# Kernel optimization log

Hardware: AMD Instinct MI355X
Metric: run time of the kernel (lower is better)

The kernel has to match this reference:

```python
import jax, jax.numpy as jnp
import numpy as np

N_NODES = 50000

def cheb_conv(x, edge_index, W, b):
    # PyG ChebConv, K=2, normalization='sym', lambda_max=2.0 (default):
    # scaled Laplacian L_hat = (2/lambda_max)*L - I = -D^{-1/2} A D^{-1/2} (zero diag).
    # Tx_0 = x, Tx_1 = L_hat @ x ; out = Tx_0 @ W[0] + Tx_1 @ W[1] + b
    src, dst = edge_index[0], edge_index[1]
    ones = jnp.ones(src.shape[0], x.dtype)
    deg = jax.ops.segment_sum(ones, src, num_segments=N_NODES)
    dinv = jnp.where(deg > 0, 1.0 / jnp.sqrt(deg), 0.0)
    norm = -dinv[src] * dinv[dst]                                   # [E]
    tx1 = jax.ops.segment_sum(x[src] * norm[:, None], dst, num_segments=N_NODES)
    return x @ W[0] + tx1 @ W[1] + b

def setup_inputs() -> dict:
    key = jax.random.key(0)
    ks = jax.random.split(key, 12)
    IN, OUT, E, P = 128, 2, 800000, 400000
    return {
        "x": jax.random.normal(ks[0], (N_NODES, IN), jnp.float32),
        "edge_index": jax.random.randint(ks[1], (2, E), 0, N_NODES),
        "E_pos": jax.random.randint(ks[2], (2, P), 0, N_NODES),
        "neg_edge_index": jax.random.randint(ks[3], (2, P), 0, N_NODES),
        "W1": jax.random.normal(ks[4], (2, IN, 300), jnp.float32) * 0.05,
        "b1": jnp.zeros((300,), jnp.float32),
        "W2": jax.random.normal(ks[5], (2, 300, 100), jnp.float32) * 0.05,
        "b2": jnp.zeros((100,), jnp.float32),
        "W3": jax.random.normal(ks[6], (2, 100, OUT), jnp.float32) * 0.05,
        "b3": jnp.zeros((OUT,), jnp.float32),
        "lin1_W": jax.random.normal(ks[7], (100, IN), jnp.float32) * 0.05,
        "lin1_b": jnp.zeros((100,), jnp.float32),
        "lin2_W": jax.random.normal(ks[8], (100, IN), jnp.float32) * 0.05,
        "lin2_b": jnp.zeros((100,), jnp.float32),
        "c1": jnp.full((1,), 0.5, jnp.float32),
        "c2": jnp.full((1,), 0.5, jnp.float32),
    }

def reference(x, edge_index, E_pos, neg_edge_index, W1, b1, W2, b2, W3, b3,
              lin1_W, lin1_b, lin2_W, lin2_b, c1, c2):
    # eval mode: F.dropout and dropout_edge are identity
    x0 = x
    h = jax.nn.relu(cheb_conv(x0, edge_index, W1, b1))
    x1 = jax.nn.relu(cheb_conv(h, edge_index, W2, b2))
    x2 = x1 + jax.nn.relu(x0 @ lin1_W.T + lin1_b)
    z = x1 + jax.nn.relu(x0 @ lin2_W.T + lin2_b)
    pos_score = jnp.sum(z[E_pos[0]] * z[E_pos[1]], axis=1)              # [P]
    pos_loss = -jnp.mean(jnp.log(jax.nn.sigmoid(pos_score) + 1e-15))
    neg_score = jnp.sum(z[neg_edge_index[0]] * z[neg_edge_index[1]], axis=1)
    neg_loss = -jnp.mean(jnp.log(1.0 - jax.nn.sigmoid(neg_score) + 1e-15))
    r_loss = pos_loss + neg_loss
    out = cheb_conv(x2, edge_index, W3, b3)                             # [N, out_channels]
    return (out, r_loss, c1, c2)
```

## Files before the change

kernel.cpp:

```cpp
#include <hip/hip_runtime.h>
#include <math.h>


typedef unsigned short ushort_t;
typedef unsigned char u8;
typedef __attribute__((ext_vector_type(8))) __bf16 bf16x8;
typedef __attribute__((ext_vector_type(8))) short s16x8;
typedef __attribute__((ext_vector_type(4))) float f32x4;
typedef __attribute__((ext_vector_type(2))) float f32x2;

#define NB_H 256
#define HW 12500
#define PW 25000

__device__ __forceinline__ f32x4 mfma16x16x32(s16x8 a, s16x8 b, f32x4 c) {
  return __builtin_amdgcn_mfma_f32_16x16x32_bf16(
      __builtin_bit_cast(bf16x8, a), __builtin_bit_cast(bf16x8, b), c, 0, 0, 0);
}
__device__ __forceinline__ ushort_t f2bf(float f) {
  union { float f; unsigned u; } c; c.f = f;
  unsigned r = (c.u + 0x7FFFu + ((c.u >> 16) & 1u)) >> 16;
  return (ushort_t)r;
}
__device__ __forceinline__ f32x2 cvt2lo(unsigned u) {
  return __builtin_amdgcn_cvt_pk_f32_fp8((int)u, false);
}
__device__ __forceinline__ f32x2 cvt2hi(unsigned u) {
  return __builtin_amdgcn_cvt_pk_f32_fp8((int)u, true);
}
__device__ __forceinline__ u8 f2fp8(float f) {
  return (u8)(__builtin_amdgcn_cvt_pk_fp8_f32(f, 0.f, 0, false) & 0xff);
}

template<int VAR, int NT, int KTOT>
__global__ __launch_bounds__(256) void gemm_mfma(
    const ushort_t* __restrict__ A0, const ushort_t* __restrict__ A1,
    const ushort_t* __restrict__ Wt,
    const float* __restrict__ bias0, const float* __restrict__ bias1,
    const float* __restrict__ x1,
    const float* __restrict__ W3c, const float* __restrict__ b3c,
    void* __restrict__ out0, void* __restrict__ out1,
    float* __restrict__ t0g, float* __restrict__ t1g, int M)
{
  constexpr int NF = NT / 32;
  __shared__ __align__(16) ushort_t As[64 * 40];
  __shared__ __align__(16) ushort_t Bs[NT * 40];
  __shared__ float w3s[400];
  const int tid  = threadIdx.x;
  const int lane = tid & 63, w = tid >> 6;
  const int m0 = blockIdx.x * 64;
  const int wm = (w & 1) * 32, wn = (w >> 1) * (NT / 2);
  if (VAR == 2) { for (int i = tid; i < 400; i += 256) w3s[i] = W3c[i]; }
  f32x4 acc[2][NF];
#pragma unroll
  for (int i = 0; i < 2; ++i)
#pragma unroll
    for (int j = 0; j < NF; ++j) acc[i][j] = (f32x4){0.f, 0.f, 0.f, 0.f};

  for (int k0 = 0; k0 < KTOT; k0 += 32) {
    {
      const int r = tid >> 2, c8 = (tid & 3) * 8;
      const int gm = m0 + r;
      uint4 v = {0u, 0u, 0u, 0u};
      if (gm < M) {
        const ushort_t* srcp;
        if (VAR == 0) srcp = (k0 < 128) ? A0 + (size_t)gm * 128 + k0 + c8
                                        : A1 + (size_t)gm * 128 + (k0 - 128) + c8;
        else if (VAR == 1) srcp = A0 + (size_t)gm * 320 + k0 + c8;
        else srcp = A0 + (size_t)gm * 128 + k0 + c8;
        v = *(const uint4*)srcp;
      }
      *(uint4*)&As[r * 40 + c8] = v;
    }
    {
      const int c8 = (tid & 3) * 8;
#pragma unroll
      for (int i = 0; i < (NT * 4 + 255) / 256; ++i) {
        const int r = (tid >> 2) + i * 64;
        if (r < NT)
          *(uint4*)&Bs[r * 40 + c8] = *(const uint4*)(Wt + (size_t)r * KTOT + k0 + c8);
      }
    }
    __syncthreads();
    s16x8 af[2], bfr[NF];
#pragma unroll
    for (int mi = 0; mi < 2; ++mi)
      af[mi] = *(const s16x8*)&As[(wm + mi * 16 + (lane & 15)) * 40 + (lane >> 4) * 8];
#pragma unroll
    for (int ni = 0; ni < NF; ++ni)
      bfr[ni] = *(const s16x8*)&Bs[(wn + ni * 16 + (lane & 15)) * 40 + (lane >> 4) * 8];
#pragma unroll
    for (int mi = 0; mi < 2; ++mi)
#pragma unroll
      for (int ni = 0; ni < NF; ++ni)
        acc[mi][ni] = mfma16x16x32(af[mi], bfr[ni], acc[mi][ni]);
    __syncthreads();
  }

  if (VAR == 2) {
#pragma unroll
    for (int mi = 0; mi < 2; ++mi)
#pragma unroll
      for (int r = 0; r < 4; ++r) {
        const int gRow = m0 + wm + mi * 16 + ((lane >> 4) << 2) + r;
        float p0 = 0.f, p1 = 0.f, p2 = 0.f, p3 = 0.f;
#pragma unroll
        for (int ni = 0; ni < NF; ++ni) {
          const int col = wn + ni * 16 + (lane & 15);
          const float v = acc[mi][ni][r];
          if (gRow < M) {
            if (col < 100) {
              const float x2v = x1[(size_t)gRow * 128 + col] + fmaxf(v + bias0[col], 0.f);
              p0 = fmaf(x2v, w3s[col * 2 + 0], p0);
              p1 = fmaf(x2v, w3s[col * 2 + 1], p1);
              p2 = fmaf(x2v, w3s[200 + col * 2 + 0], p2);
              p3 = fmaf(x2v, w3s[200 + col * 2 + 1], p3);
            } else if (col < 200) {
              const int c = col - 100;
              ((u8*)out1)[(size_t)gRow * 128 + c] =
                  f2fp8(x1[(size_t)gRow * 128 + c] + fmaxf(v + bias1[c], 0.f));
            }
          }
        }
        if (wn == 0) {
#pragma unroll
          for (int off = 8; off; off >>= 1) {
            p0 += __shfl_down(p0, off, 16);
            p1 += __shfl_down(p1, off, 16);
            p2 += __shfl_down(p2, off, 16);
            p3 += __shfl_down(p3, off, 16);
          }
          if ((lane & 15) == 0 && gRow < M) {
            t0g[(size_t)gRow * 2 + 0] = p0 + b3c[0];
            t0g[(size_t)gRow * 2 + 1] = p1 + b3c[1];
            t1g[(size_t)gRow * 2 + 0] = p2;
            t1g[(size_t)gRow * 2 + 1] = p3;
          }
        }
      }
  } else {
#pragma unroll
    for (int mi = 0; mi < 2; ++mi)
#pragma unroll
      for (int ni = 0; ni < NF; ++ni)
#pragma unroll
        for (int r = 0; r < 4; ++r) {
          const int gRow = m0 + wm + mi * 16 + ((lane >> 4) << 2) + r;
          const int col  = wn + ni * 16 + (lane & 15);
          if (gRow >= M) continue;
          const float v = acc[mi][ni][r];
          if (VAR == 0) {
            ushort_t* h = (ushort_t*)out0;
            h[(size_t)gRow * 320 + col] = (col < 300) ? f2bf(fmaxf(v + bias0[col], 0.f))
                                                      : (ushort_t)0;
          } else {
            if (col < 100) ((float*)out0)[(size_t)gRow * 128 + col] = v + bias0[col];
            else if (col < 200) ((u8*)out1)[(size_t)gRow * 128 + (col - 100)] = f2fp8(v);
          }
        }
  }
}

__global__ void pack_cvt(const float* __restrict__ x, ushort_t* __restrict__ xb,
                         u8* __restrict__ xf8, int n4,
                         const float* __restrict__ W1, const float* __restrict__ W2,
                         const float* __restrict__ l1W, const float* __restrict__ l2W,
                         ushort_t* __restrict__ W1t, ushort_t* __restrict__ W2t,
                         ushort_t* __restrict__ Wlt) {
  const int i = blockIdx.x * 256 + threadIdx.x;
  if (i < n4) {
    const float4 v = ((const float4*)x)[i];
    ushort4 o; o.x = f2bf(v.x); o.y = f2bf(v.y); o.z = f2bf(v.z); o.w = f2bf(v.w);
    ((ushort4*)xb)[i] = o;
    int p = 0;
    p = __builtin_amdgcn_cvt_pk_fp8_f32(v.x, v.y, p, false);
    p = __builtin_amdgcn_cvt_pk_fp8_f32(v.z, v.w, p, true);
    ((unsigned*)xf8)[i] = (unsigned)p;
    return;
  }
  const int j = i - n4;
  if (j < 81920) {
    const int n = j >> 8, k = j & 255;
    float v = 0.f;
    if (n < 300) v = (k < 128) ? W1[k * 300 + n] : W1[38400 + (k - 128) * 300 + n];
    W1t[j] = f2bf(v);
  } else if (j < 153600) {
    const int jj = j - 81920;
    const int n = jj / 320, k = jj - n * 320;
    float v = 0.f;
    if (n < 200 && k < 300) v = W2[(n < 100 ? 0 : 30000) + k * 100 + (n % 100)];
    W2t[jj] = f2bf(v);
  } else if (j < 182272) {
    const int jj = j - 153600;
    const int n = jj >> 7, k = jj & 127;
    float v = 0.f;
    if (n < 100) v = l1W[n * 128 + k];
    else if (n < 200) v = l2W[(n - 100) * 128 + k];
    Wlt[jj] = f2bf(v);
  }
}

__global__ __launch_bounds__(256) void hist2(
    const int* __restrict__ src, const int* __restrict__ dst, int E, int M,
    unsigned* __restrict__ partS, unsigned* __restrict__ partD,
    ushort_t* __restrict__ rank)
{
  __shared__ unsigned hist[HW];
  const int b = blockIdx.x;
  const int cs = (E + NB_H - 1) / NB_H;
  const int e0 = b * cs;
  const int e1 = (e0 + cs < E) ? e0 + cs : E;
  for (int isD = 0; isD < 2; ++isD) {
    const int* keys = isD ? dst : src;
    unsigned* part = isD ? partD : partS;
    for (int r = 0; r < 2; ++r) {
      const int klo = r * 2 * HW;
      for (int i = threadIdx.x; i < HW; i += 256) hist[i] = 0;
      __syncthreads();
      for (int e = e0 + threadIdx.x; e < e1; e += 256) {
        const int k = keys[e] - klo;
        if ((unsigned)k < (unsigned)(2 * HW)) {
          const unsigned old = atomicAdd(&hist[k >> 1], (k & 1) ? 0x10000u : 1u);
          if (isD) rank[e] = (ushort_t)((old >> ((k & 1) * 16)) & 0xffffu);
        }
      }
      __syncthreads();
      for (int i = threadIdx.x; i < HW; i += 256)
        part[(size_t)b * PW + r * HW + i] = hist[i];
      __syncthreads();
    }
  }
}

__global__ __launch_bounds__(256) void reduce_base2(
    const unsigned* __restrict__ partS, unsigned* __restrict__ partD,
    float* __restrict__ dinv, int* __restrict__ cnt, int M)
{
  const int t = blockIdx.x * 256 + threadIdx.x;
  if (t < PW) {
    const int i = t;
    unsigned ssum = 0;
    for (int b = 0; b < NB_H; b += 8) {
      unsigned v[8];
#pragma unroll
      for (int q = 0; q < 8; ++q) v[q] = partS[(size_t)(b + q) * PW + i];
#pragma unroll
      for (int q = 0; q < 8; ++q) ssum += v[q];
    }
    const int k = 2 * i;
    const unsigned s0 = ssum & 0xffffu, s1 = ssum >> 16;
    if (k < M) dinv[k] = s0 ? 1.f / sqrtf((float)s0) : 0.f;
    if (k + 1 < M) dinv[k + 1] = s1 ? 1.f / sqrtf((float)s1) : 0.f;
  } else if (t < 2 * PW) {
    const int i = t - PW;
    unsigned run = 0;
    for (int b = 0; b < NB_H; b += 8) {
      unsigned v[8], pre[8];
#pragma unroll
      for (int q = 0; q < 8; ++q) v[q] = partD[(size_t)(b + q) * PW + i];
#pragma unroll
      for (int q = 0; q < 8; ++q) { pre[q] = run; run += v[q]; }
#pragma unroll
      for (int q = 0; q < 8; ++q) partD[(size_t)(b + q) * PW + i] = pre[q];
    }
    const int k = 2 * i;
    if (k < M) cnt[k] = (int)(run & 0xffffu);
    if (k + 1 < M) cnt[k + 1] = (int)(run >> 16);
  }
}

__global__ void scan_local(const int* __restrict__ cnt, int* __restrict__ ptr,
                           int* __restrict__ bsum, int n)
{
  __shared__ int tmp[256];
  const int i = blockIdx.x * 256 + threadIdx.x;
  const int v = (i < n) ? cnt[i] : 0;
  tmp[threadIdx.x] = v;
  __syncthreads();
  for (int off = 1; off < 256; off <<= 1) {
    const int t = (threadIdx.x >= off) ? tmp[threadIdx.x - off] : 0;
    __syncthreads();
    tmp[threadIdx.x] += t;
    __syncthreads();
  }
  if (i < n) ptr[i] = tmp[threadIdx.x] - v;
  if (threadIdx.x == 255) bsum[blockIdx.x] = tmp[255];
}
__global__ void scan_bsum(int* __restrict__ bsum, int nb, float* __restrict__ accs) {
  __shared__ int tmp[256];
  if (threadIdx.x < 2) accs[threadIdx.x] = 0.f;
  const int v = (threadIdx.x < nb) ? bsum[threadIdx.x] : 0;
  tmp[threadIdx.x] = v;
  __syncthreads();
  for (int off = 1; off < 256; off <<= 1) {
    const int t = (threadIdx.x >= off) ? tmp[threadIdx.x - off] : 0;
    __syncthreads();
    tmp[threadIdx.x] += t;
    __syncthreads();
  }
  if (threadIdx.x < nb) bsum[threadIdx.x] = tmp[threadIdx.x] - v;
}
__global__ void scan_add(int* __restrict__ ptr, const int* __restrict__ bsum, int n, int E) {
  const int i = blockIdx.x * 256 + threadIdx.x;
  if (i < n) ptr[i] += bsum[blockIdx.x];
  if (i == 0) ptr[n] = E;
}

__global__ void fill_csr2(const int* __restrict__ src, const int* __restrict__ dst,
                          const float* __restrict__ dinv, const int* __restrict__ ptr,
                          const unsigned* __restrict__ base32,
                          const ushort_t* __restrict__ rank,
                          int2* __restrict__ csr, int E)
{
  const int e = blockIdx.x * 256 + threadIdx.x;
  if (e >= E) return;
  const int cs = (E + NB_H - 1) / NB_H;
  const int b = e / cs;
  const int s = src[e], d = dst[e];
  const unsigned bv = base32[(size_t)b * PW + (d >> 1)];
  const int base = (int)((bv >> ((d & 1) * 16)) & 0xffffu);
  const int pos = ptr[d] + base + (int)rank[e];
  const float w = -dinv[s] * dinv[d];
  csr[pos] = make_int2(s, __float_as_int(w));
}

#define ACCV(u, ww) { f32x2 t; \
  t = cvt2lo(u.x); a[0]  = fmaf(ww, t.x, a[0]);  a[1]  = fmaf(ww, t.y, a[1]);  \
  t = cvt2hi(u.x); a[2]  = fmaf(ww, t.x, a[2]);  a[3]  = fmaf(ww, t.y, a[3]);  \
  t = cvt2lo(u.y); a[4]  = fmaf(ww, t.x, a[4]);  a[5]  = fmaf(ww, t.y, a[5]);  \
  t = cvt2hi(u.y); a[6]  = fmaf(ww, t.x, a[6]);  a[7]  = fmaf(ww, t.y, a[7]);  \
  t = cvt2lo(u.z); a[8]  = fmaf(ww, t.x, a[8]);  a[9]  = fmaf(ww, t.y, a[9]);  \
  t = cvt2hi(u.z); a[10] = fmaf(ww, t.x, a[10]); a[11] = fmaf(ww, t.y, a[11]); \
  t = cvt2lo(u.w); a[12] = fmaf(ww, t.x, a[12]); a[13] = fmaf(ww, t.y, a[13]); \
  t = cvt2hi(u.w); a[14] = fmaf(ww, t.x, a[14]); a[15] = fmaf(ww, t.y, a[15]); }

__global__ __launch_bounds__(256) void gather128e(
    const u8* __restrict__ xf8, ushort_t* __restrict__ txb,
    const int* __restrict__ ptr, const int2* __restrict__ csr, int M)
{
  const int node = (blockIdx.x * 256 + threadIdx.x) >> 3;
  const int sub  = threadIdx.x & 7;
  if (node >= M) return;
  const int beg = ptr[node], end = ptr[node + 1];
  float a[16] = {};
  int p = beg;
  for (; p + 8 <= end; p += 8) {
    int2 e[8];
#pragma unroll
    for (int q = 0; q < 8; ++q) e[q] = csr[p + q];
    uint4 v[8];
#pragma unroll
    for (int q = 0; q < 8; ++q)
      v[q] = *(const uint4*)(xf8 + (size_t)e[q].x * 128 + sub * 16);
#pragma unroll
    for (int q = 0; q < 8; ++q) { const float wq = __int_as_float(e[q].y); ACCV(v[q], wq) }
  }
  for (; p < end; ++p) {
    const int2 eq = csr[p]; const float wq = __int_as_float(eq.y);
    const uint4 v = *(const uint4*)(xf8 + (size_t)eq.x * 128 + sub * 16);
    ACCV(v, wq)
  }
  uint4 o1, o2;
  o1.x = (unsigned)f2bf(a[0])  | ((unsigned)f2bf(a[1])  << 16);
  o1.y = (unsigned)f2bf(a[2])  | ((unsigned)f2bf(a[3])  << 16);
  o1.z = (unsigned)f2bf(a[4])  | ((unsigned)f2bf(a[5])  << 16);
  o1.w = (unsigned)f2bf(a[6])  | ((unsigned)f2bf(a[7])  << 16);
  o2.x = (unsigned)f2bf(a[8])  | ((unsigned)f2bf(a[9])  << 16);
  o2.y = (unsigned)f2bf(a[10]) | ((unsigned)f2bf(a[11]) << 16);
  o2.z = (unsigned)f2bf(a[12]) | ((unsigned)f2bf(a[13]) << 16);
  o2.w = (unsigned)f2bf(a[14]) | ((unsigned)f2bf(a[15]) << 16);
  ushort_t* dstp = txb + (size_t)node * 128 + sub * 16;
  *(uint4*)dstp = o1;
  *(uint4*)(dstp + 8) = o2;
}

__global__ __launch_bounds__(256) void gather100e_x1(
    const u8* __restrict__ Brh, float* __restrict__ Ar,
    const int* __restrict__ ptr, const int2* __restrict__ csr, int M)
{
  const int node = (blockIdx.x * 256 + threadIdx.x) >> 3;
  const int sub  = threadIdx.x & 7;
  if (node >= M) return;
  const int beg = ptr[node], end = ptr[node + 1];
  float a[16] = {};
  int p = beg;
  for (; p + 8 <= end; p += 8) {
    int2 e[8];
#pragma unroll
    for (int q = 0; q < 8; ++q) e[q] = csr[p + q];
    uint4 v[8];
#pragma unroll
    for (int q = 0; q < 8; ++q)
      v[q] = *(const uint4*)(Brh + (size_t)e[q].x * 128 + sub * 16);
#pragma unroll
    for (int q = 0; q < 8; ++q) { const float wq = __int_as_float(e[q].y); ACCV(v[q], wq) }
  }
  for (; p < end; ++p) {
    const int2 eq = csr[p]; const float wq = __int_as_float(eq.y);
    const uint4 v = *(const uint4*)(Brh + (size_t)eq.x * 128 + sub * 16);
    ACCV(v, wq)
  }
  float* dstp = Ar + (size_t)node * 128 + sub * 16;
#pragma unroll
  for (int q = 0; q < 4; ++q) {
    float4 b = *(const float4*)(dstp + q * 4);
    b.x = fmaxf(b.x + a[q * 4 + 0], 0.f);
    b.y = fmaxf(b.y + a[q * 4 + 1], 0.f);
    b.z = fmaxf(b.z + a[q * 4 + 2], 0.f);
    b.w = fmaxf(b.w + a[q * 4 + 3], 0.f);
    *(float4*)(dstp + q * 4) = b;
  }
}
#undef ACCV

__device__ __forceinline__ void maskrow(uint4& r, int sub) {
  if (sub >= 6) { r.y = 0u; r.z = 0u; r.w = 0u; if (sub == 7) r.x = 0u; }
}
#define DOTV(uu, vv, s) { f32x2 p_, q_; \
  p_ = cvt2lo(uu.x); q_ = cvt2lo(vv.x); s = fmaf(p_.x, q_.x, s); s = fmaf(p_.y, q_.y, s); \
  p_ = cvt2hi(uu.x); q_ = cvt2hi(vv.x); s = fmaf(p_.x, q_.x, s); s = fmaf(p_.y, q_.y, s); \
  p_ = cvt2lo(uu.y); q_ = cvt2lo(vv.y); s = fmaf(p_.x, q_.x, s); s = fmaf(p_.y, q_.y, s); \
  p_ = cvt2hi(uu.y); q_ = cvt2hi(vv.y); s = fmaf(p_.x, q_.x, s); s = fmaf(p_.y, q_.y, s); \
  p_ = cvt2lo(uu.z); q_ = cvt2lo(vv.z); s = fmaf(p_.x, q_.x, s); s = fmaf(p_.y, q_.y, s); \
  p_ = cvt2hi(uu.z); q_ = cvt2hi(vv.z); s = fmaf(p_.x, q_.x, s); s = fmaf(p_.y, q_.y, s); \
  p_ = cvt2lo(uu.w); q_ = cvt2lo(vv.w); s = fmaf(p_.x, q_.x, s); s = fmaf(p_.y, q_.y, s); \
  p_ = cvt2hi(uu.w); q_ = cvt2hi(vv.w); s = fmaf(p_.x, q_.x, s); s = fmaf(p_.y, q_.y, s); }

__global__ __launch_bounds__(256) void loss_fp8(
    const u8* __restrict__ zf8, const int* __restrict__ ep,
    const int* __restrict__ en, int P, float* __restrict__ acc)
{
  __shared__ float red[8];
  const int tid = threadIdx.x;
  const int lane = tid & 63, wib = tid >> 6;
  const int sub = tid & 7;
  const int slot0 = blockIdx.x * 32 + (tid >> 3);
  const int step = gridDim.x * 32;
  float tp = 0.f, tn = 0.f;
  int g = slot0;
  for (; g + 3 * step < 2 * P; g += 4 * step) {
    int neg[4], na[4], nb[4];
#pragma unroll
    for (int q = 0; q < 4; ++q) {
      const int gq = g + q * step;
      neg[q] = (gq >= P);
      const int p = neg[q] ? gq - P : gq;
      const int* ia = neg[q] ? en : ep;
      na[q] = ia[p]; nb[q] = ia[P + p];
    }
    uint4 ra[4], rb[4];
#pragma unroll
    for (int q = 0; q < 4; ++q) {
      ra[q] = *(const uint4*)(zf8 + (size_t)na[q] * 128 + sub * 16);
      rb[q] = *(const uint4*)(zf8 + (size_t)nb[q] * 128 + sub * 16);
      maskrow(ra[q], sub); maskrow(rb[q], sub);
    }
    float s[4] = {0.f, 0.f, 0.f, 0.f};
#pragma unroll
    for (int q = 0; q < 4; ++q) DOTV(ra[q], rb[q], s[q])
#pragma unroll
    for (int off = 4; off; off >>= 1) {
#pragma unroll
      for (int q = 0; q < 4; ++q) s[q] += __shfl_down(s[q], off, 8);
    }
    if (sub == 0) {
#pragma unroll
      for (int q = 0; q < 4; ++q) {
        const float sig = 1.f / (1.f + expf(-s[q]));
        if (neg[q]) tn += logf(1.f - sig + 1e-15f); else tp += logf(sig + 1e-15f);
      }
    }
  }
  for (; g < 2 * P; g += step) {
    const int neg = (g >= P);
    const int p = neg ? g - P : g;
    const int* ia = neg ? en : ep;
    const int na = ia[p], nb = ia[P + p];
    uint4 ra = *(const uint4*)(zf8 + (size_t)na * 128 + sub * 16);
    uint4 rb = *(const uint4*)(zf8 + (size_t)nb * 128 + sub * 16);
    maskrow(ra, sub); maskrow(rb, sub);
    float s = 0.f;
    DOTV(ra, rb, s)
#pragma unroll
    for (int off = 4; off; off >>= 1) s += __shfl_down(s, off, 8);
    if (sub == 0) {
      const float sig = 1.f / (1.f + expf(-s));
      if (neg) tn += logf(1.f - sig + 1e-15f); else tp += logf(sig + 1e-15f);
    }
  }
  tp += __shfl_down(tp, 32, 64); tn += __shfl_down(tn, 32, 64);
  tp += __shfl_down(tp, 16, 64); tn += __shfl_down(tn, 16, 64);
  tp += __shfl_down(tp, 8, 64);  tn += __shfl_down(tn, 8, 64);
  if (lane == 0) { red[wib] = tp; red[4 + wib] = tn; }
  __syncthreads();
  if (tid == 0) {
    atomicAdd(acc + 0, red[0] + red[1] + red[2] + red[3]);
    atomicAdd(acc + 1, red[4] + red[5] + red[6] + red[7]);
  }
}
#undef DOTV

__global__ void gather2_final(
    const float* __restrict__ t1, const float* __restrict__ t0,
    const int* __restrict__ ptr, const int2* __restrict__ csr,
    const float* __restrict__ accs,
    const float* __restrict__ c1, const float* __restrict__ c2,
    float* __restrict__ out, int M, float invP)
{
  const int i = blockIdx.x * blockDim.x + threadIdx.x;
  if (i < M) {
    float a0 = 0.f, a1 = 0.f;
    const int beg = ptr[i], end = ptr[i + 1];
    int p = beg;
    for (; p + 4 <= end; p += 4) {
      const int2 e0 = csr[p], e1 = csr[p + 1], e2 = csr[p + 2], e3 = csr[p + 3];
      const float w0 = __int_as_float(e0.y), w1 = __int_as_float(e1.y);
      const float w2 = __int_as_float(e2.y), w3 = __int_as_float(e3.y);
      const float2 v0 = *(const float2*)(t1 + (size_t)e0.x * 2);
      const float2 v1 = *(const float2*)(t1 + (size_t)e1.x * 2);
      const float2 v2 = *(const float2*)(t1 + (size_t)e2.x * 2);
      const float2 v3 = *(const float2*)(t1 + (size_t)e3.x * 2);
      a0 = fmaf(w0, v0.x, a0); a1 = fmaf(w0, v0.y, a1);
      a0 = fmaf(w1, v1.x, a0); a1 = fmaf(w1, v1.y, a1);
      a0 = fmaf(w2, v2.x, a0); a1 = fmaf(w2, v2.y, a1);
      a0 = fmaf(w3, v3.x, a0); a1 = fmaf(w3, v3.y, a1);
    }
    for (; p < end; ++p) {
      const int2 eq = csr[p]; const float wq = __int_as_float(eq.y);
      const float2 v = *(const float2*)(t1 + (size_t)eq.x * 2);
      a0 = fmaf(wq, v.x, a0); a1 = fmaf(wq, v.y, a1);
    }
    const float2 base = *(const float2*)(t0 + (size_t)i * 2);
    *(float2*)(out + (size_t)i * 2) = make_float2(base.x + a0, base.y + a1);
  }
  if (i == 0) {
    out[2 * M + 0] = -(accs[0] + accs[1]) * invP;
    out[2 * M + 1] = c1[0];
    out[2 * M + 2] = c2[0];
  }
}

extern "C" void kernel_launch(void* const* d_in, const int* in_sizes, int n_in,
                              void* d_out, int out_size, void* d_ws, size_t ws_size,
                              hipStream_t stream)
{
  const float* x   = (const float*)d_in[0];
  const int*   ei  = (const int*)d_in[1];
  const int*   ep  = (const int*)d_in[2];
  const int*   en  = (const int*)d_in[3];
  const float* W1  = (const float*)d_in[4];
  const float* b1  = (const float*)d_in[5];
  const float* W2  = (const float*)d_in[6];
  const float* b2  = (const float*)d_in[7];
  const float* W3  = (const float*)d_in[8];
  const float* b3  = (const float*)d_in[9];
  const float* l1W = (const float*)d_in[10];
  const float* l1b = (const float*)d_in[11];
  const float* l2W = (const float*)d_in[12];
  const float* l2b = (const float*)d_in[13];
  const float* c1  = (const float*)d_in[14];
  const float* c2  = (const float*)d_in[15];
  float* out = (float*)d_out;

  const int M = in_sizes[0] / 128;
  const int E = in_sizes[1] / 2;
  const int P = in_sizes[2] / 2;
  const int* src = ei;
  const int* dst = ei + E;
  const int nb_scan = (M + 255) / 256;

  float* ws = (float*)d_ws;
  size_t o = 0;
  float*    dinv = ws + o;            o += 50176;
  int*      cnt  = (int*)(ws + o);    o += (size_t)M;
  int*      ptr  = (int*)(ws + o);    o += (size_t)M + 8;
  int*      bsum = (int*)(ws + o);    o += 256;
  int2*     csr  = (int2*)(ws + o);   o += (size_t)E * 2;
  ushort_t* rank = (ushort_t*)(ws + o); o += (size_t)E / 2;
  ushort_t* xb   = (ushort_t*)(ws + o); o += (size_t)M * 64;
  u8*       xf8  = (u8*)(ws + o);     o += (size_t)M * 32;
  ushort_t* tx0b = (ushort_t*)(ws + o); o += (size_t)M * 64;
  ushort_t* W1t  = (ushort_t*)(ws + o); o += 40960;
  ushort_t* W2t  = (ushort_t*)(ws + o); o += 35840;
  ushort_t* Wlt  = (ushort_t*)(ws + o); o += 14336;
  ushort_t* h    = (ushort_t*)(ws + o); o += (size_t)M * 160;
  float*    Ar   = ws + o;            o += (size_t)M * 128;
  u8*       Brh  = (u8*)(ws + o);     o += (size_t)M * 32;
  u8*       zf8  = (u8*)(ws + o);     o += (size_t)M * 32;
  float*    t0   = ws + o;            o += (size_t)M * 2;
  float*    t1   = ws + o;            o += (size_t)M * 2;
  float*    accs = ws + o;            o += 8;
  unsigned* partS = (unsigned*)h;
  unsigned* partD = (unsigned*)Ar;

  const int n4 = M * 32;
  pack_cvt<<<(n4 + 182272 + 255) / 256, 256, 0, stream>>>(
      x, xb, xf8, n4, W1, W2, l1W, l2W, W1t, W2t, Wlt);

  hist2<<<NB_H, 256, 0, stream>>>(src, dst, E, M, partS, partD, rank);
  reduce_base2<<<(2 * PW + 255) / 256, 256, 0, stream>>>(partS, partD, dinv, cnt, M);
  scan_local<<<nb_scan, 256, 0, stream>>>(cnt, ptr, bsum, M);
  scan_bsum<<<1, 256, 0, stream>>>(bsum, nb_scan, accs);
  scan_add<<<nb_scan, 256, 0, stream>>>(ptr, bsum, M, E);
  fill_csr2<<<(E + 255) / 256, 256, 0, stream>>>(src, dst, dinv, ptr, partD, rank, csr, E);

  const int gB = (M + 63) / 64;
  const int gE8 = (M * 8 + 255) / 256;

  gather128e<<<gE8, 256, 0, stream>>>(xf8, tx0b, ptr, csr, M);
  gemm_mfma<0, 320, 256><<<gB, 256, 0, stream>>>(
      xb, tx0b, W1t, b1, nullptr, nullptr, nullptr, nullptr, h, nullptr, nullptr, nullptr, M);

  gemm_mfma<1, 224, 320><<<gB, 256, 0, stream>>>(
      h, nullptr, W2t, b2, nullptr, nullptr, nullptr, nullptr, Ar, Brh, nullptr, nullptr, M);
  gather100e_x1<<<gE8, 256, 0, stream>>>(Brh, Ar, ptr, csr, M);

  gemm_mfma<2, 224, 128><<<gB, 256, 0, stream>>>(
      xb, nullptr, Wlt, l1b, l2b, Ar , W3, b3, nullptr, zf8, t0, t1, M);

  loss_fp8<<<2048, 256, 0, stream>>>(zf8, ep, en, P, accs);

  gather2_final<<<(M + 255) / 256, 256, 0, stream>>>(t1, t0, ptr, csr,
                                                     accs, c1, c2, out, M, 1.0f / (float)P);
}
```

Measured before the change: 476.9 us.

## Split fp8 feature tables into two 64-byte column planes for cache-resident gathers

Stores the fp8 copies of x, Brh and z as two planes of 64 bytes per node instead of 128-byte rows. The sparse gathers and the loss dot-products then run as two passes, one per plane, so each pass touches half the working set and has a better chance of staying in L2/MALL. The loss is split into a partial-sum pass that writes per-pair scores and a second pass that adds the rest and applies the log-sigmoid. This adds extra kernel launches, reads the CSR and edge indices twice, and writes and reads a 2P-float scratch buffer.

```diff
diff --git a/kernel.cpp b/kernel.cpp
--- a/kernel.cpp
+++ b/kernel.cpp
@@ -50,6 +50,7 @@
   const int lane = tid & 63, w = tid >> 6;
   const int m0 = blockIdx.x * 64;
   const int wm = (w & 1) * 32, wn = (w >> 1) * (NT / 2);
+  const size_t pstride = (size_t)M * 64;
   if (VAR == 2) { for (int i = tid; i < 400; i += 256) w3s[i] = W3c[i]; }
   f32x4 acc[2][NF];
 #pragma unroll
@@ -117,7 +118,8 @@
               p3 = fmaf(x2v, w3s[200 + col * 2 + 1], p3);
             } else if (col < 200) {
               const int c = col - 100;
-              ((u8*)out1)[(size_t)gRow * 128 + c] =
+              const int pl = (c >= 64);
+              ((u8*)out1)[pl * pstride + (size_t)gRow * 64 + (c - pl * 64)] =
                   f2fp8(x1[(size_t)gRow * 128 + c] + fmaxf(v + bias1[c], 0.f));
             }
           }
@@ -155,14 +157,18 @@
                                                       : (ushort_t)0;
           } else {
             if (col < 100) ((float*)out0)[(size_t)gRow * 128 + col] = v + bias0[col];
-            else if (col < 200) ((u8*)out1)[(size_t)gRow * 128 + (col - 100)] = f2fp8(v);
+            else if (col < 200) {
+              const int c = col - 100;
+              const int pl = (c >= 64);
+              ((u8*)out1)[pl * pstride + (size_t)gRow * 64 + (c - pl * 64)] = f2fp8(v);
+            }
           }
         }
   }
 }
 
 __global__ void pack_cvt(const float* __restrict__ x, ushort_t* __restrict__ xb,
-                         u8* __restrict__ xf8, int n4,
+                         u8* __restrict__ xf8, int n4, int M,
                          const float* __restrict__ W1, const float* __restrict__ W2,
                          const float* __restrict__ l1W, const float* __restrict__ l2W,
                          ushort_t* __restrict__ W1t, ushort_t* __restrict__ W2t,
@@ -175,7 +181,10 @@
     int p = 0;
     p = __builtin_amdgcn_cvt_pk_fp8_f32(v.x, v.y, p, false);
     p = __builtin_amdgcn_cvt_pk_fp8_f32(v.z, v.w, p, true);
-    ((unsigned*)xf8)[i] = (unsigned)p;
+    const int row = i >> 5, g = i & 31;
+    const int col = g * 4;
+    const int pl = col >> 6, off = col & 63;
+    *(unsigned*)(xf8 + (size_t)pl * M * 64 + (size_t)row * 64 + off) = (unsigned)p;
     return;
   }
   const int j = i - n4;
@@ -334,12 +343,13 @@
   t = cvt2lo(u.w); a[12] = fmaf(ww, t.x, a[12]); a[13] = fmaf(ww, t.y, a[13]); \
   t = cvt2hi(u.w); a[14] = fmaf(ww, t.x, a[14]); a[15] = fmaf(ww, t.y, a[15]); }
 
-__global__ __launch_bounds__(256) void gather128e(
-    const u8* __restrict__ xf8, ushort_t* __restrict__ txb,
+template<int PLANE>
+__global__ __launch_bounds__(256) void gather128p(
+    const u8* __restrict__ xp, ushort_t* __restrict__ txb,
     const int* __restrict__ ptr, const int2* __restrict__ csr, int M)
 {
-  const int node = (blockIdx.x * 256 + threadIdx.x) >> 3;
-  const int sub  = threadIdx.x & 7;
+  const int node = (blockIdx.x * 256 + threadIdx.x) >> 2;
+  const int sub  = threadIdx.x & 3;
   if (node >= M) return;
   const int beg = ptr[node], end = ptr[node + 1];
   float a[16] = {};
@@ -351,13 +361,13 @@
     uint4 v[8];
 #pragma unroll
     for (int q = 0; q < 8; ++q)
-      v[q] = *(const uint4*)(xf8 + (size_t)e[q].x * 128 + sub * 16);
+      v[q] = *(const uint4*)(xp + (size_t)e[q].x * 64 + sub * 16);
 #pragma unroll
     for (int q = 0; q < 8; ++q) { const float wq = __int_as_float(e[q].y); ACCV(v[q], wq) }
   }
   for (; p < end; ++p) {
     const int2 eq = csr[p]; const float wq = __int_as_float(eq.y);
-    const uint4 v = *(const uint4*)(xf8 + (size_t)eq.x * 128 + sub * 16);
+    const uint4 v = *(const uint4*)(xp + (size_t)eq.x * 64 + sub * 16);
     ACCV(v, wq)
   }
   uint4 o1, o2;
@@ -369,17 +379,18 @@
   o2.y = (unsigned)f2bf(a[10]) | ((unsigned)f2bf(a[11]) << 16);
   o2.z = (unsigned)f2bf(a[12]) | ((unsigned)f2bf(a[13]) << 16);
   o2.w = (unsigned)f2bf(a[14]) | ((unsigned)f2bf(a[15]) << 16);
-  ushort_t* dstp = txb + (size_t)node * 128 + sub * 16;
+  ushort_t* dstp = txb + (size_t)node * 128 + PLANE * 64 + sub * 16;
   *(uint4*)dstp = o1;
   *(uint4*)(dstp + 8) = o2;
 }
 
-__global__ __launch_bounds__(256) void gather100e_x1(
-    const u8* __restrict__ Brh, float* __restrict__ Ar,
+template<int PLANE>
+__global__ __launch_bounds__(256) void gather100p_x1(
+    const u8* __restrict__ Bp, float* __restrict__ Ar,
     const int* __restrict__ ptr, const int2* __restrict__ csr, int M)
 {
-  const int node = (blockIdx.x * 256 + threadIdx.x) >> 3;
-  const int sub  = threadIdx.x & 7;
+  const int node = (blockIdx.x * 256 + threadIdx.x) >> 2;
+  const int sub  = threadIdx.x & 3;
   if (node >= M) return;
   const int beg = ptr[node], end = ptr[node + 1];
   float a[16] = {};
@@ -391,16 +402,16 @@
     uint4 v[8];
 #pragma unroll
     for (int q = 0; q < 8; ++q)
-      v[q] = *(const uint4*)(Brh + (size_t)e[q].x * 128 + sub * 16);
+      v[q] = *(const uint4*)(Bp + (size_t)e[q].x * 64 + sub * 16);
 #pragma unroll
     for (int q = 0; q < 8; ++q) { const float wq = __int_as_float(e[q].y); ACCV(v[q], wq) }
   }
   for (; p < end; ++p) {
     const int2 eq = csr[p]; const float wq = __int_as_float(eq.y);
-    const uint4 v = *(const uint4*)(Brh + (size_t)eq.x * 128 + sub * 16);
+    const uint4 v = *(const uint4*)(Bp + (size_t)eq.x * 64 + sub * 16);
     ACCV(v, wq)
   }
-  float* dstp = Ar + (size_t)node * 128 + sub * 16;
+  float* dstp = Ar + (size_t)node * 128 + PLANE * 64 + sub * 16;
 #pragma unroll
   for (int q = 0; q < 4; ++q) {
     float4 b = *(const float4*)(dstp + q * 4);
@@ -413,9 +424,6 @@
 }
 #undef ACCV
 
-__device__ __forceinline__ void maskrow(uint4& r, int sub) {
-  if (sub >= 6) { r.y = 0u; r.z = 0u; r.w = 0u; if (sub == 7) r.x = 0u; }
-}
 #define DOTV(uu, vv, s) { f32x2 p_, q_; \
   p_ = cvt2lo(uu.x); q_ = cvt2lo(vv.x); s = fmaf(p_.x, q_.x, s); s = fmaf(p_.y, q_.y, s); \
   p_ = cvt2hi(uu.x); q_ = cvt2hi(vv.x); s = fmaf(p_.x, q_.x, s); s = fmaf(p_.y, q_.y, s); \
@@ -426,71 +434,93 @@
   p_ = cvt2lo(uu.w); q_ = cvt2lo(vv.w); s = fmaf(p_.x, q_.x, s); s = fmaf(p_.y, q_.y, s); \
   p_ = cvt2hi(uu.w); q_ = cvt2hi(vv.w); s = fmaf(p_.x, q_.x, s); s = fmaf(p_.y, q_.y, s); }
 
-__global__ __launch_bounds__(256) void loss_fp8(
-    const u8* __restrict__ zf8, const int* __restrict__ ep,
-    const int* __restrict__ en, int P, float* __restrict__ acc)
-{
-  __shared__ float red[8];
+__global__ __launch_bounds__(256) void loss_p0(
+    const u8* __restrict__ zp, const int* __restrict__ ep,
+    const int* __restrict__ en, int P, float* __restrict__ sp)
+{
   const int tid = threadIdx.x;
-  const int lane = tid & 63, wib = tid >> 6;
-  const int sub = tid & 7;
-  const int slot0 = blockIdx.x * 32 + (tid >> 3);
-  const int step = gridDim.x * 32;
-  float tp = 0.f, tn = 0.f;
+  const int sub = tid & 3;
+  const int slot0 = blockIdx.x * 64 + (tid >> 2);
+  const int step = gridDim.x * 64;
   int g = slot0;
   for (; g + 3 * step < 2 * P; g += 4 * step) {
-    int neg[4], na[4], nb[4];
+    int na[4], nb[4];
 #pragma unroll
     for (int q = 0; q < 4; ++q) {
       const int gq = g + q * step;
-      neg[q] = (gq >= P);
-      const int p = neg[q] ? gq - P : gq;
-      const int* ia = neg[q] ? en : ep;
+      const int neg = (gq >= P);
+      const int p = neg ? gq - P : gq;
+      const int* ia = neg ? en : ep;
       na[q] = ia[p]; nb[q] = ia[P + p];
     }
     uint4 ra[4], rb[4];
 #pragma unroll
     for (int q = 0; q < 4; ++q) {
-      ra[q] = *(const uint4*)(zf8 + (size_t)na[q] * 128 + sub * 16);
-      rb[q] = *(const uint4*)(zf8 + (size_t)nb[q] * 128 + sub * 16);
-      maskrow(ra[q], sub); maskrow(rb[q], sub);
+      ra[q] = *(const uint4*)(zp + (size_t)na[q] * 64 + sub * 16);
+      rb[q] = *(const uint4*)(zp + (size_t)nb[q] * 64 + sub * 16);
     }
     float s[4] = {0.f, 0.f, 0.f, 0.f};
 #pragma unroll
     for (int q = 0; q < 4; ++q) DOTV(ra[q], rb[q], s[q])
 #pragma unroll
-    for (int off = 4; off; off >>= 1) {
-#pragma unroll
-      for (int q = 0; q < 4; ++q) s[q] += __shfl_down(s[q], off, 8);
-    }
-    if (sub == 0) {
-#pragma unroll
-      for (int q = 0; q < 4; ++q) {
-        const float sig = 1.f / (1.f + expf(-s[q]));
-        if (neg[q]) tn += logf(1.f - sig + 1e-15f); else tp += logf(sig + 1e-15f);
-      }
-    }
+    for (int off = 2; off; off >>= 1)
+#pragma unroll
+      for (int q = 0; q < 4; ++q) s[q] += __shfl_down(s[q], off, 4);
+    if (sub == 0)
+#pragma unroll
+      for (int q = 0; q < 4; ++q) sp[g + q * step] = s[q];
   }
   for (; g < 2 * P; g += step) {
     const int neg = (g >= P);
     const int p = neg ? g - P : g;
     const int* ia = neg ? en : ep;
     const int na = ia[p], nb = ia[P + p];
-    uint4 ra = *(const uint4*)(zf8 + (size_t)na * 128 + sub * 16);
-    uint4 rb = *(const uint4*)(zf8 + (size_t)nb * 128 + sub * 16);
-    maskrow(ra, sub); maskrow(rb, sub);
+    const uint4 ra = *(const uint4*)(zp + (size_t)na * 64 + sub * 16);
+    const uint4 rb = *(const uint4*)(zp + (size_t)nb * 64 + sub * 16);
     float s = 0.f;
     DOTV(ra, rb, s)
 #pragma unroll
-    for (int off = 4; off; off >>= 1) s += __shfl_down(s, off, 8);
+    for (int off = 2; off; off >>= 1) s += __shfl_down(s, off, 4);
+    if (sub == 0) sp[g] = s;
+  }
+}
+
+__global__ __launch_bounds__(256) void loss_p1(
+    const u8* __restrict__ zp1, const int* __restrict__ ep,
+    const int* __restrict__ en, int P, const float* __restrict__ sp,
+    float* __restrict__ acc)
+{
+  __shared__ float red[8];
+  const int tid = threadIdx.x;
+  const int lane = tid & 63, wib = tid >> 6;
+  const int sub = tid & 3;
+  const int slot0 = blockIdx.x * 64 + (tid >> 2);
+  const int step = gridDim.x * 64;
+  float tp = 0.f, tn = 0.f;
+  for (int g = slot0; g < 2 * P; g += step) {
+    const int neg = (g >= P);
+    const int p = neg ? g - P : g;
+    const int* ia = neg ? en : ep;
+    const int na = ia[p], nb = ia[P + p];
+    float s = 0.f;
+    if (sub < 3) {
+      uint4 ra = *(const uint4*)(zp1 + (size_t)na * 64 + sub * 16);
+      uint4 rb = *(const uint4*)(zp1 + (size_t)nb * 64 + sub * 16);
+      if (sub == 2) { ra.y = ra.z = ra.w = 0u; rb.y = rb.z = rb.w = 0u; }
+      DOTV(ra, rb, s)
+    }
+#pragma unroll
+    for (int off = 2; off; off >>= 1) s += __shfl_down(s, off, 4);
     if (sub == 0) {
-      const float sig = 1.f / (1.f + expf(-s));
+      const float st = s + sp[g];
+      const float sig = 1.f / (1.f + expf(-st));
       if (neg) tn += logf(1.f - sig + 1e-15f); else tp += logf(sig + 1e-15f);
     }
   }
   tp += __shfl_down(tp, 32, 64); tn += __shfl_down(tn, 32, 64);
   tp += __shfl_down(tp, 16, 64); tn += __shfl_down(tn, 16, 64);
   tp += __shfl_down(tp, 8, 64);  tn += __shfl_down(tn, 8, 64);
+  tp += __shfl_down(tp, 4, 64);  tn += __shfl_down(tn, 4, 64);
   if (lane == 0) { red[wib] = tp; red[4 + wib] = tn; }
   __syncthreads();
   if (tid == 0) {
@@ -587,15 +617,17 @@
   float*    Ar   = ws + o;            o += (size_t)M * 128;
   u8*       Brh  = (u8*)(ws + o);     o += (size_t)M * 32;
   u8*       zf8  = (u8*)(ws + o);     o += (size_t)M * 32;
+  float*    sp   = ws + o;            o += (size_t)2 * P;
   float*    t0   = ws + o;            o += (size_t)M * 2;
   float*    t1   = ws + o;            o += (size_t)M * 2;
   float*    accs = ws + o;            o += 8;
   unsigned* partS = (unsigned*)h;
   unsigned* partD = (unsigned*)Ar;
+  const size_t pstride = (size_t)M * 64;
 
   const int n4 = M * 32;
   pack_cvt<<<(n4 + 182272 + 255) / 256, 256, 0, stream>>>(
-      x, xb, xf8, n4, W1, W2, l1W, l2W, W1t, W2t, Wlt);
+      x, xb, xf8, n4, M, W1, W2, l1W, l2W, W1t, W2t, Wlt);
 
   hist2<<<NB_H, 256, 0, stream>>>(src, dst, E, M, partS, partD, rank);
   reduce_base2<<<(2 * PW + 255) / 256, 256, 0, stream>>>(partS, partD, dinv, cnt, M);
@@ -605,20 +637,23 @@
   fill_csr2<<<(E + 255) / 256, 256, 0, stream>>>(src, dst, dinv, ptr, partD, rank, csr, E);
 
   const int gB = (M + 63) / 64;
-  const int gE8 = (M * 8 + 255) / 256;
-
-  gather128e<<<gE8, 256, 0, stream>>>(xf8, tx0b, ptr, csr, M);
+  const int gP4 = (M * 4 + 255) / 256;
+
+  gather128p<0><<<gP4, 256, 0, stream>>>(xf8, tx0b, ptr, csr, M);
+  gather128p<1><<<gP4, 256, 0, stream>>>(xf8 + pstride, tx0b, ptr, csr, M);
   gemm_mfma<0, 320, 256><<<gB, 256, 0, stream>>>(
       xb, tx0b, W1t, b1, nullptr, nullptr, nullptr, nullptr, h, nullptr, nullptr, nullptr, M);
 
   gemm_mfma<1, 224, 320><<<gB, 256, 0, stream>>>(
       h, nullptr, W2t, b2, nullptr, nullptr, nullptr, nullptr, Ar, Brh, nullptr, nullptr, M);
-  gather100e_x1<<<gE8, 256, 0, stream>>>(Brh, Ar, ptr, csr, M);
+  gather100p_x1<0><<<gP4, 256, 0, stream>>>(Brh, Ar, ptr, csr, M);
+  gather100p_x1<1><<<gP4, 256, 0, stream>>>(Brh + pstride, Ar, ptr, csr, M);
 
   gemm_mfma<2, 224, 128><<<gB, 256, 0, stream>>>(
       xb, nullptr, Wlt, l1b, l2b, Ar , W3, b3, nullptr, zf8, t0, t1, M);
 
-  loss_fp8<<<2048, 256, 0, stream>>>(zf8, ep, en, P, accs);
+  loss_p0<<<2048, 256, 0, stream>>>(zf8, ep, en, P, sp);
+  loss_p1<<<2048, 256, 0, stream>>>(zf8 + pstride, ep, en, P, sp, accs);
 
   gather2_final<<<(M + 255) / 256, 256, 0, stream>>>(t1, t0, ptr, csr,
                                                      accs, c1, c2, out, M, 1.0f / (float)P);
```

Measured after the change: 502.3 us. 1.05x slower.
